# Performance work log

Measured on AMD Instinct MI355X. Metric: run time of the kernel, lower is better.

The kernel has to match this reference:

```python
import jax, jax.numpy as jnp
import numpy as np

DIM = 1024
HEADS = 16
DIM_HEAD = 64
INNER = HEADS * DIM_HEAD  # 1024
EPS = 1e-5


def setup_inputs() -> dict:
    key = jax.random.key(0)
    ks = jax.random.split(key, 5)
    x = jax.random.normal(ks[0], (4, 2048, DIM), dtype=jnp.float32)
    ln_gamma = jnp.ones((DIM,), dtype=jnp.float32)
    ln_beta = jnp.zeros((DIM,), dtype=jnp.float32)
    # nn.Linear weights ~ U(-1/sqrt(fan_in), 1/sqrt(fan_in)); stored as (out, in) in torch,
    # here kept as (in, out) for x @ W.
    lim = 1.0 / np.sqrt(DIM)
    w_qkv = jax.random.uniform(ks[1], (DIM, 3 * INNER), minval=-lim, maxval=lim, dtype=jnp.float32)
    lim2 = 1.0 / np.sqrt(INNER)
    w_out = jax.random.uniform(ks[2], (INNER, DIM), minval=-lim2, maxval=lim2, dtype=jnp.float32)
    return {"x": x, "ln_gamma": ln_gamma, "ln_beta": ln_beta, "w_qkv": w_qkv, "w_out": w_out}


def reference(x, ln_gamma, ln_beta, w_qkv, w_out):
    b, n, d = x.shape
    # LayerNorm
    mu = jnp.mean(x, axis=-1, keepdims=True)
    var = jnp.mean(jnp.square(x - mu), axis=-1, keepdims=True)
    xn = (x - mu) * jax.lax.rsqrt(var + EPS) * ln_gamma + ln_beta
    # QKV projection
    qkv = xn @ w_qkv  # (b, n, 3*inner)
    q, k, v = jnp.split(qkv, 3, axis=-1)
    def to_heads(t):
        return t.reshape(b, n, HEADS, DIM_HEAD).transpose(0, 2, 1, 3)  # (b,h,n,dh)
    q, k, v = to_heads(q), to_heads(k), to_heads(v)
    scale = DIM_HEAD ** -0.5
    scores = jnp.einsum('bhqd,bhkd->bhqk', q, k) * scale
    causal = jnp.tril(jnp.ones((n, n), dtype=bool))
    scores = jnp.where(causal, scores, -jnp.inf)
    probs = jax.nn.softmax(scores, axis=-1)
    out = jnp.einsum('bhqk,bhkd->bhqd', probs, v)
    out = out.transpose(0, 2, 1, 3).reshape(b, n, INNER)
    return out @ w_out
```

## Files before the change

kernel.cpp:

```cpp
#include <hip/hip_runtime.h>
#include <hip/hip_bf16.h>

#define DIM 1024
#define HEADS 16
#define DH 64
#define SEQ 2048
#define BATCH 4
#define ROWS (BATCH * SEQ)
#define NQKV (3 * DIM)

typedef __attribute__((ext_vector_type(8))) __bf16 bf16x8;
typedef __attribute__((ext_vector_type(4))) __bf16 bf16x4;
typedef __attribute__((ext_vector_type(4))) float f32x4;

__device__ inline void gload16(const void* g, void* l) {
  __builtin_amdgcn_global_load_lds(
      (const __attribute__((address_space(1))) void*)g,
      (__attribute__((address_space(3))) void*)l, 16, 0, 0);
}

__device__ inline float fast_exp2(float x) {
#if __has_builtin(__builtin_amdgcn_exp2f)
  return __builtin_amdgcn_exp2f(x);
#else
  return exp2f(x);
#endif
}

__global__ __launch_bounds__(256) void ln_kernel(
    const float* __restrict__ x, const float* __restrict__ gamma,
    const float* __restrict__ beta, __bf16* __restrict__ xnb) {
  const int row = blockIdx.x;
  const int tid = threadIdx.x;
  const float4* xr = (const float4*)(x + (size_t)row * DIM);
  float4 v = xr[tid];
  float s1 = v.x + v.y + v.z + v.w;
  float s2 = v.x * v.x + v.y * v.y + v.z * v.z + v.w * v.w;
#pragma unroll
  for (int d = 32; d > 0; d >>= 1) {
    s1 += __shfl_xor(s1, d);
    s2 += __shfl_xor(s2, d);
  }
  __shared__ float red1[4], red2[4];
  const int wave = tid >> 6, lane = tid & 63;
  if (lane == 0) { red1[wave] = s1; red2[wave] = s2; }
  __syncthreads();
  s1 = red1[0] + red1[1] + red1[2] + red1[3];
  s2 = red2[0] + red2[1] + red2[2] + red2[3];
  const float mean = s1 * (1.0f / DIM);
  const float var = s2 * (1.0f / DIM) - mean * mean;
  const float rstd = rsqrtf(var + 1e-5f);
  float4 g = ((const float4*)gamma)[tid];
  float4 b = ((const float4*)beta)[tid];
  bf16x4 o;
  o[0] = (__bf16)((v.x - mean) * rstd * g.x + b.x);
  o[1] = (__bf16)((v.y - mean) * rstd * g.y + b.y);
  o[2] = (__bf16)((v.z - mean) * rstd * g.z + b.z);
  o[3] = (__bf16)((v.w - mean) * rstd * g.w + b.w);
  *(bf16x4*)(xnb + (size_t)row * DIM + tid * 4) = o;
}

__global__ __launch_bounds__(256) void transpose_cast(
    const float* __restrict__ in, __bf16* __restrict__ outT, int rows, int cols) {
  __shared__ float tile[32][33];
  const int tx = threadIdx.x & 31, ty = threadIdx.x >> 5;
  const int c0 = blockIdx.x * 32, r0 = blockIdx.y * 32;
#pragma unroll
  for (int rr = ty; rr < 32; rr += 8)
    tile[rr][tx] = in[(size_t)(r0 + rr) * cols + c0 + tx];
  __syncthreads();
#pragma unroll
  for (int rr = ty; rr < 32; rr += 8)
    outT[(size_t)(c0 + rr) * rows + r0 + tx] = (__bf16)tile[tx][rr];
}

template <int MODE>
__global__ __launch_bounds__(256) void gemm128(
    const __bf16* __restrict__ A, const __bf16* __restrict__ Bt, int K, int N,
    float* __restrict__ Cout, __bf16* __restrict__ qb, __bf16* __restrict__ kb,
    __bf16* __restrict__ vtb) {
  __shared__ __bf16 As[2][128 * 32];
  __shared__ __bf16 Bs[2][128 * 32];
  const int tid = threadIdx.x;
  const int wave = tid >> 6, lane = tid & 63;
  const int quad = lane >> 4, l16 = lane & 15;
  const int wm = wave >> 1, wn = wave & 1;
  const size_t tileM = (size_t)blockIdx.x * 128;
  const size_t tileN = (size_t)blockIdx.y * 128;
  const int sel = (MODE == 1) ? (int)(tileN >> 10) : 0;
  const bool vmode = (MODE == 1) && (sel == 2);

  f32x4 acc[4][4];
#pragma unroll
  for (int i = 0; i < 4; ++i)
#pragma unroll
    for (int j = 0; j < 4; ++j) acc[i][j] = (f32x4){0.f, 0.f, 0.f, 0.f};

  const int sr = lane >> 2;
  const int sc = lane & 3;
  const int ck = (l16 >> 1) & 3;

  const __bf16* Abase = A + tileM * (size_t)K;
  const __bf16* Bbase = Bt + tileN * (size_t)K;

  auto stage = [&](int buf, int k0) {
#pragma unroll
    for (int p = 0; p < 2; ++p) {
      const int rbase = p * 64 + wave * 16;
      const int row = rbase + sr;
      const int gc = (sc ^ ((row >> 1) & 3)) << 3;
      gload16(Abase + (size_t)row * K + k0 + gc, &As[buf][rbase * 32]);
      gload16(Bbase + (size_t)row * K + k0 + gc, &Bs[buf][rbase * 32]);
    }
  };

  const int NIT = K >> 5;
  stage(0, 0);
  for (int it = 0; it < NIT; ++it) {
    __syncthreads();
    if (it + 1 < NIT) stage((it + 1) & 1, (it + 1) << 5);
    const int buf = it & 1;
    bf16x8 af[4], bfr[4];
#pragma unroll
    for (int mt = 0; mt < 4; ++mt)
      af[mt] =
          *(const bf16x8*)&As[buf][(wm * 64 + mt * 16 + l16) * 32 + ((quad ^ ck) << 3)];
#pragma unroll
    for (int nt = 0; nt < 4; ++nt)
      bfr[nt] =
          *(const bf16x8*)&Bs[buf][(wn * 64 + nt * 16 + l16) * 32 + ((quad ^ ck) << 3)];
    if (vmode) {
#pragma unroll
      for (int mt = 0; mt < 4; ++mt)
#pragma unroll
        for (int nt = 0; nt < 4; ++nt)
          acc[mt][nt] = __builtin_amdgcn_mfma_f32_16x16x32_bf16(af[mt], bfr[nt],
                                                                acc[mt][nt], 0, 0, 0);
    } else {
#pragma unroll
      for (int mt = 0; mt < 4; ++mt)
#pragma unroll
        for (int nt = 0; nt < 4; ++nt)
          acc[mt][nt] = __builtin_amdgcn_mfma_f32_16x16x32_bf16(bfr[nt], af[mt],
                                                                acc[mt][nt], 0, 0, 0);
    }
  }

  if (MODE == 0) {
#pragma unroll
    for (int mt = 0; mt < 4; ++mt) {
      const size_t m = tileM + wm * 64 + mt * 16 + l16;
#pragma unroll
      for (int nt = 0; nt < 4; ++nt) {
        const size_t n0 = tileN + wn * 64 + nt * 16 + quad * 4;
        *(f32x4*)&Cout[m * (size_t)N + n0] = acc[mt][nt];
      }
    }
  } else if (sel < 2) {
    __bf16* dst = (sel == 0) ? qb : kb;
#pragma unroll
    for (int mt = 0; mt < 4; ++mt) {
      const size_t m = tileM + wm * 64 + mt * 16 + l16;
      const int b = (int)(m >> 11), seq = (int)(m & 2047);
#pragma unroll
      for (int nt = 0; nt < 4; ++nt) {
        const int c = (int)(tileN & 1023) + wn * 64 + nt * 16 + quad * 4;
        const int head = c >> 6, dh = c & 63;
        bf16x4 pk;
#pragma unroll
        for (int r = 0; r < 4; ++r) pk[r] = (__bf16)acc[mt][nt][r];
        *(bf16x4*)&dst[(((size_t)b * HEADS + head) * SEQ + seq) * DH + dh] = pk;
      }
    }
  } else {
#pragma unroll
    for (int nt = 0; nt < 4; ++nt) {
      const int c = (int)(tileN & 1023) + wn * 64 + nt * 16 + l16;
      const int head = c >> 6, dh = c & 63;
#pragma unroll
      for (int mt = 0; mt < 4; ++mt) {
        const size_t m0 = tileM + wm * 64 + mt * 16 + quad * 4;
        const int b = (int)(m0 >> 11), seq = (int)(m0 & 2047);
        bf16x4 pk;
#pragma unroll
        for (int r = 0; r < 4; ++r) pk[r] = (__bf16)acc[mt][nt][r];
        *(bf16x4*)&vtb[(((size_t)b * HEADS + head) * DH + dh) * SEQ + seq] = pk;
      }
    }
  }
}

__global__ __launch_bounds__(256, 4) void attn_kernel(
    const __bf16* __restrict__ qb, const __bf16* __restrict__ kb,
    const __bf16* __restrict__ vtb, __bf16* __restrict__ ob) {
  const int bh = blockIdx.x;
  const int by = blockIdx.y;
  const int tid = threadIdx.x;
  const int wave = tid >> 6, lane = tid & 63;
  const int quad = lane >> 4, l16 = lane & 15;

  __shared__ __bf16 Ks[2][64 * 64];
  __shared__ __bf16 Vs[2][64 * 64];
  __shared__ __bf16 Ps[4][16 * 36];

  const __bf16* kg = kb + (size_t)bh * SEQ * DH;
  const __bf16* vg = vtb + (size_t)bh * DH * SEQ;

  const int i1 = by, i2 = 31 - by;
  const int T = 33;

  const int kr = lane >> 3, kc = lane & 7;

  auto stage = [&](int buf, int j) {
#pragma unroll
    for (int p = 0; p < 2; ++p) {
      const int rbase = wave * 16 + p * 8;
      const int row = rbase + kr;
      gload16(kg + (size_t)(j * 64 + row) * DH + ((kc ^ (row & 7)) << 3),
              &Ks[buf][rbase * 64]);
      gload16(vg + (size_t)row * SEQ + j * 64 + ((kc ^ (row & 7)) << 3),
              &Vs[buf][rbase * 64]);
    }
  };

  const float QSCALE = 0.125f * 1.44269504088896f;
  bf16x8 qf[2];
  auto load_q = [&](int i) {
    const __bf16* qbase = qb + ((size_t)bh * SEQ + (size_t)i * 64 + wave * 16) * DH;
#pragma unroll
    for (int ks = 0; ks < 2; ++ks) {
      bf16x8 v = *(const bf16x8*)(qbase + l16 * DH + ks * 32 + quad * 8);
#pragma unroll
      for (int e = 0; e < 8; ++e) v[e] = (__bf16)((float)v[e] * QSCALE);
      qf[ks] = v;
    }
  };

  float m_i, l_i;
  f32x4 o_acc[4];
  auto reset_state = [&]() {
    m_i = -1e30f;
    l_i = 0.f;
#pragma unroll
    for (int md = 0; md < 4; ++md) o_acc[md] = (f32x4){0.f, 0.f, 0.f, 0.f};
  };
  const int b_out = bh >> 4, h_out = bh & 15;
  auto epilogue = [&](int i) {
    float lsum = l_i;
    lsum += __shfl_xor(lsum, 16);
    lsum += __shfl_xor(lsum, 32);
    const float inv = __builtin_amdgcn_rcpf(lsum);
    const int seq = i * 64 + wave * 16 + l16;
    __bf16* dst = ob + ((size_t)b_out * SEQ + seq) * DIM + h_out * DH;
#pragma unroll
    for (int md = 0; md < 4; ++md) {
      bf16x4 pk;
#pragma unroll
      for (int r = 0; r < 4; ++r) pk[r] = (__bf16)(o_acc[md][r] * inv);
      *(bf16x4*)(dst + md * 16 + quad * 4) = pk;
    }
  };

  load_q(i1);
  reset_state();
  stage(0, 0);

  for (int t = 0; t < T; ++t) {
    __syncthreads();
    if (t + 1 < T) {
      const int jn = (t + 1 <= by) ? (t + 1) : (t - by);
      stage((t + 1) & 1, jn);
    }
    const int buf = t & 1;
    const int i = (t <= by) ? i1 : i2;
    const int j = (t <= by) ? t : (t - by - 1);
    const bool diag = (j == i);

    f32x4 sa[4];
#pragma unroll
    for (int nt = 0; nt < 4; ++nt) sa[nt] = (f32x4){0.f, 0.f, 0.f, 0.f};
#pragma unroll
    for (int nt = 0; nt < 4; ++nt)
#pragma unroll
      for (int ks = 0; ks < 2; ++ks) {
        bf16x8 kf = *(const bf16x8*)&Ks[buf][(nt * 16 + l16) * 64 +
                                            (((ks * 4 + quad) ^ (l16 & 7)) << 3)];
        sa[nt] = __builtin_amdgcn_mfma_f32_16x16x32_bf16(kf, qf[ks], sa[nt], 0, 0, 0);
      }

    if (diag) {
      const int qrl = wave * 16 + l16;
#pragma unroll
      for (int nt = 0; nt < 4; ++nt)
#pragma unroll
        for (int r = 0; r < 4; ++r) {
          const int kvl = nt * 16 + quad * 4 + r;
          if (kvl > qrl) sa[nt][r] = -1e30f;
        }
    }

    {
      float mx = -1e30f;
#pragma unroll
      for (int nt = 0; nt < 4; ++nt)
#pragma unroll
        for (int r = 0; r < 4; ++r) mx = fmaxf(mx, sa[nt][r]);
      mx = fmaxf(mx, __shfl_xor(mx, 16));
      mx = fmaxf(mx, __shfl_xor(mx, 32));
      const float mnew = fmaxf(m_i, mx);
      const float alpha = fast_exp2(m_i - mnew);
      m_i = mnew;
      float rs = 0.f;
#pragma unroll
      for (int nt = 0; nt < 4; ++nt)
#pragma unroll
        for (int r = 0; r < 4; ++r) {
          const float p = fast_exp2(sa[nt][r] - mnew);
          sa[nt][r] = p;
          rs += p;
        }
      l_i = l_i * alpha + rs;
#pragma unroll
      for (int md = 0; md < 4; ++md)
#pragma unroll
        for (int r = 0; r < 4; ++r) o_acc[md][r] *= alpha;
    }

#pragma unroll
    for (int c = 0; c < 2; ++c) {
#pragma unroll
      for (int ntl = 0; ntl < 2; ++ntl) {
        const int nt = c * 2 + ntl;
        bf16x4 pk;
#pragma unroll
        for (int r = 0; r < 4; ++r) pk[r] = (__bf16)sa[nt][r];
        *(bf16x4*)&Ps[wave][l16 * 36 + ntl * 16 + quad * 4] = pk;
      }
      bf16x8 pf = *(const bf16x8*)&Ps[wave][l16 * 36 + quad * 8];
#pragma unroll
      for (int md = 0; md < 4; ++md) {
        bf16x8 vf = *(const bf16x8*)&Vs[buf][(md * 16 + l16) * 64 +
                                            (((c * 4 + quad) ^ (l16 & 7)) << 3)];
        o_acc[md] = __builtin_amdgcn_mfma_f32_16x16x32_bf16(vf, pf, o_acc[md], 0, 0, 0);
      }
    }

    if (t == by) {
      epilogue(i1);
      reset_state();
      load_q(i2);
    }
  }
  epilogue(i2);
}

extern "C" void kernel_launch(void* const* d_in, const int* in_sizes, int n_in,
                              void* d_out, int out_size, void* d_ws, size_t ws_size,
                              hipStream_t stream) {
  const float* x = (const float*)d_in[0];
  const float* gamma = (const float*)d_in[1];
  const float* beta = (const float*)d_in[2];
  const float* w_qkv = (const float*)d_in[3];
  const float* w_out = (const float*)d_in[4];
  float* out = (float*)d_out;

  char* ws = (char*)d_ws;
  const size_t MB = 1024 * 1024;
  __bf16* xnb = (__bf16*)ws;
  __bf16* wqkvT = (__bf16*)(ws + 16 * MB);
  __bf16* woutT = (__bf16*)(ws + 24 * MB);
  __bf16* qbuf = (__bf16*)(ws + 32 * MB);
  __bf16* kbuf = (__bf16*)(ws + 48 * MB);
  __bf16* vtbuf = (__bf16*)(ws + 64 * MB);
  __bf16* attnb = xnb;

  ln_kernel<<<ROWS, 256, 0, stream>>>(x, gamma, beta, xnb);
  transpose_cast<<<dim3(NQKV / 32, DIM / 32), 256, 0, stream>>>(w_qkv, wqkvT, DIM, NQKV);
  transpose_cast<<<dim3(DIM / 32, DIM / 32), 256, 0, stream>>>(w_out, woutT, DIM, DIM);
  gemm128<1><<<dim3(ROWS / 128, NQKV / 128), 256, 0, stream>>>(
      xnb, wqkvT, DIM, NQKV, nullptr, qbuf, kbuf, vtbuf);
  attn_kernel<<<dim3(BATCH * HEADS, 16), 256, 0, stream>>>(qbuf, kbuf, vtbuf, attnb);
  gemm128<0><<<dim3(ROWS / 128, DIM / 128), 256, 0, stream>>>(
      attnb, woutT, DIM, DIM, out, nullptr, nullptr, nullptr);
}
```

Before: 285.0 us.

## Rewrite projection GEMMs as 256x256 tiles with 4-stage pipeline and XCD swizzle

Replaces the 128x128 two-buffer GEMM with a 256x256 tile using 512 threads, four LDS stages with explicit vmcnt waits, and staggered A/B staging split around two MFMA halves. Block indices are remapped so consecutive tiles land on the same XCD for L2 reuse, and setprio raises MFMA priority. The larger tile raises arithmetic intensity, but LDS use (128KB) and register pressure grow and the grid shrinks to 384/128 blocks, which risks poor occupancy and tail effects.

```diff
diff --git a/kernel.cpp b/kernel.cpp
--- a/kernel.cpp
+++ b/kernel.cpp
@@ -75,81 +75,145 @@
 }
 
 template <int MODE>
-__global__ __launch_bounds__(256) void gemm128(
-    const __bf16* __restrict__ A, const __bf16* __restrict__ Bt, int K, int N,
-    float* __restrict__ Cout, __bf16* __restrict__ qb, __bf16* __restrict__ kb,
-    __bf16* __restrict__ vtb) {
-  __shared__ __bf16 As[2][128 * 32];
-  __shared__ __bf16 Bs[2][128 * 32];
+__global__ __launch_bounds__(512, 2) void gemm256(
+    const __bf16* __restrict__ A, const __bf16* __restrict__ Bt, const int K,
+    const int N, float* __restrict__ Cout, __bf16* __restrict__ qb,
+    __bf16* __restrict__ kb, __bf16* __restrict__ vtb) {
+  __shared__ __bf16 As[4][256 * 32];
+  __shared__ __bf16 Bs[4][256 * 32];
   const int tid = threadIdx.x;
   const int wave = tid >> 6, lane = tid & 63;
   const int quad = lane >> 4, l16 = lane & 15;
-  const int wm = wave >> 1, wn = wave & 1;
-  const size_t tileM = (size_t)blockIdx.x * 128;
-  const size_t tileN = (size_t)blockIdx.y * 128;
+  const int wm = wave >> 2, wn = wave & 3;
+
+  const int cpx = gridDim.x >> 3;
+  const int wg = ((int)blockIdx.x & 7) * cpx + ((int)blockIdx.x >> 3);
+  const int MT = ROWS / 256;
+  const size_t tileM = (size_t)(wg % MT) * 256;
+  const size_t tileN = (size_t)(wg / MT) * 256;
   const int sel = (MODE == 1) ? (int)(tileN >> 10) : 0;
   const bool vmode = (MODE == 1) && (sel == 2);
 
-  f32x4 acc[4][4];
-#pragma unroll
-  for (int i = 0; i < 4; ++i)
+  f32x4 acc[8][4];
+#pragma unroll
+  for (int i = 0; i < 8; ++i)
 #pragma unroll
     for (int j = 0; j < 4; ++j) acc[i][j] = (f32x4){0.f, 0.f, 0.f, 0.f};
 
   const int sr = lane >> 2;
   const int sc = lane & 3;
   const int ck = (l16 >> 1) & 3;
+  const int coff = (quad ^ ck) << 3;
 
   const __bf16* Abase = A + tileM * (size_t)K;
   const __bf16* Bbase = Bt + tileN * (size_t)K;
 
-  auto stage = [&](int buf, int k0) {
+  auto stageA = [&](int buf, int k0) {
 #pragma unroll
     for (int p = 0; p < 2; ++p) {
-      const int rbase = p * 64 + wave * 16;
+      const int rbase = (wave * 2 + p) * 16;
       const int row = rbase + sr;
       const int gc = (sc ^ ((row >> 1) & 3)) << 3;
       gload16(Abase + (size_t)row * K + k0 + gc, &As[buf][rbase * 32]);
+    }
+  };
+  auto stageB = [&](int buf, int k0) {
+#pragma unroll
+    for (int p = 0; p < 2; ++p) {
+      const int rbase = (wave * 2 + p) * 16;
+      const int row = rbase + sr;
+      const int gc = (sc ^ ((row >> 1) & 3)) << 3;
       gload16(Bbase + (size_t)row * K + k0 + gc, &Bs[buf][rbase * 32]);
     }
   };
 
-  const int NIT = K >> 5;
-  stage(0, 0);
-  for (int it = 0; it < NIT; ++it) {
-    __syncthreads();
-    if (it + 1 < NIT) stage((it + 1) & 1, (it + 1) << 5);
-    const int buf = it & 1;
-    bf16x8 af[4], bfr[4];
-#pragma unroll
-    for (int mt = 0; mt < 4; ++mt)
-      af[mt] =
-          *(const bf16x8*)&As[buf][(wm * 64 + mt * 16 + l16) * 32 + ((quad ^ ck) << 3)];
+  const int NT = K >> 5;
+  stageA(0, 0);
+  stageB(0, 0);
+  stageA(1, 32);
+  stageB(1, 32);
+  stageA(2, 64);
+  stageB(2, 64);
+
+  for (int t = 0; t < NT; ++t) {
+    if (t < NT - 2)
+      asm volatile("s_waitcnt vmcnt(8)" ::: "memory");
+    else if (t < NT - 1)
+      asm volatile("s_waitcnt vmcnt(4)" ::: "memory");
+    else
+      asm volatile("s_waitcnt vmcnt(0)" ::: "memory");
+    __builtin_amdgcn_s_barrier();
+    asm volatile("" ::: "memory");
+    __builtin_amdgcn_sched_barrier(0);
+
+    const int buf = t & 3;
+    const int sbuf = (t + 3) & 3;
+    const bool do_stage = (t + 3 < NT);
+    const int k3 = (t + 3) << 5;
+
+    if (do_stage) stageA(sbuf, k3);
+    bf16x8 bfr[4];
 #pragma unroll
     for (int nt = 0; nt < 4; ++nt)
-      bfr[nt] =
-          *(const bf16x8*)&Bs[buf][(wn * 64 + nt * 16 + l16) * 32 + ((quad ^ ck) << 3)];
-    if (vmode) {
+      bfr[nt] = *(const bf16x8*)&Bs[buf][(wn * 64 + nt * 16 + l16) * 32 + coff];
+    {
+      bf16x8 af[4];
 #pragma unroll
       for (int mt = 0; mt < 4; ++mt)
-#pragma unroll
-        for (int nt = 0; nt < 4; ++nt)
-          acc[mt][nt] = __builtin_amdgcn_mfma_f32_16x16x32_bf16(af[mt], bfr[nt],
-                                                                acc[mt][nt], 0, 0, 0);
-    } else {
+        af[mt] = *(const bf16x8*)&As[buf][(wm * 128 + mt * 16 + l16) * 32 + coff];
+      __builtin_amdgcn_s_setprio(1);
+      if (vmode) {
+#pragma unroll
+        for (int mt = 0; mt < 4; ++mt)
+#pragma unroll
+          for (int nt = 0; nt < 4; ++nt)
+            acc[mt][nt] = __builtin_amdgcn_mfma_f32_16x16x32_bf16(
+                af[mt], bfr[nt], acc[mt][nt], 0, 0, 0);
+      } else {
+#pragma unroll
+        for (int mt = 0; mt < 4; ++mt)
+#pragma unroll
+          for (int nt = 0; nt < 4; ++nt)
+            acc[mt][nt] = __builtin_amdgcn_mfma_f32_16x16x32_bf16(
+                bfr[nt], af[mt], acc[mt][nt], 0, 0, 0);
+      }
+      __builtin_amdgcn_s_setprio(0);
+    }
+    __builtin_amdgcn_s_barrier();
+    asm volatile("" ::: "memory");
+    __builtin_amdgcn_sched_barrier(0);
+
+    if (do_stage) stageB(sbuf, k3);
+    {
+      bf16x8 af[4];
 #pragma unroll
       for (int mt = 0; mt < 4; ++mt)
-#pragma unroll
-        for (int nt = 0; nt < 4; ++nt)
-          acc[mt][nt] = __builtin_amdgcn_mfma_f32_16x16x32_bf16(bfr[nt], af[mt],
-                                                                acc[mt][nt], 0, 0, 0);
+        af[mt] =
+            *(const bf16x8*)&As[buf][(wm * 128 + (mt + 4) * 16 + l16) * 32 + coff];
+      __builtin_amdgcn_s_setprio(1);
+      if (vmode) {
+#pragma unroll
+        for (int mt = 0; mt < 4; ++mt)
+#pragma unroll
+          for (int nt = 0; nt < 4; ++nt)
+            acc[mt + 4][nt] = __builtin_amdgcn_mfma_f32_16x16x32_bf16(
+                af[mt], bfr[nt], acc[mt + 4][nt], 0, 0, 0);
+      } else {
+#pragma unroll
+        for (int mt = 0; mt < 4; ++mt)
+#pragma unroll
+          for (int nt = 0; nt < 4; ++nt)
+            acc[mt + 4][nt] = __builtin_amdgcn_mfma_f32_16x16x32_bf16(
+                bfr[nt], af[mt], acc[mt + 4][nt], 0, 0, 0);
+      }
+      __builtin_amdgcn_s_setprio(0);
     }
   }
 
   if (MODE == 0) {
 #pragma unroll
-    for (int mt = 0; mt < 4; ++mt) {
-      const size_t m = tileM + wm * 64 + mt * 16 + l16;
+    for (int mt = 0; mt < 8; ++mt) {
+      const size_t m = tileM + wm * 128 + mt * 16 + l16;
 #pragma unroll
       for (int nt = 0; nt < 4; ++nt) {
         const size_t n0 = tileN + wn * 64 + nt * 16 + quad * 4;
@@ -159,8 +223,8 @@
   } else if (sel < 2) {
     __bf16* dst = (sel == 0) ? qb : kb;
 #pragma unroll
-    for (int mt = 0; mt < 4; ++mt) {
-      const size_t m = tileM + wm * 64 + mt * 16 + l16;
+    for (int mt = 0; mt < 8; ++mt) {
+      const size_t m = tileM + wm * 128 + mt * 16 + l16;
       const int b = (int)(m >> 11), seq = (int)(m & 2047);
 #pragma unroll
       for (int nt = 0; nt < 4; ++nt) {
@@ -178,8 +242,8 @@
       const int c = (int)(tileN & 1023) + wn * 64 + nt * 16 + l16;
       const int head = c >> 6, dh = c & 63;
 #pragma unroll
-      for (int mt = 0; mt < 4; ++mt) {
-        const size_t m0 = tileM + wm * 64 + mt * 16 + quad * 4;
+      for (int mt = 0; mt < 8; ++mt) {
+        const size_t m0 = tileM + wm * 128 + mt * 16 + quad * 4;
         const int b = (int)(m0 >> 11), seq = (int)(m0 & 2047);
         bf16x4 pk;
 #pragma unroll
@@ -377,9 +441,9 @@
   ln_kernel<<<ROWS, 256, 0, stream>>>(x, gamma, beta, xnb);
   transpose_cast<<<dim3(NQKV / 32, DIM / 32), 256, 0, stream>>>(w_qkv, wqkvT, DIM, NQKV);
   transpose_cast<<<dim3(DIM / 32, DIM / 32), 256, 0, stream>>>(w_out, woutT, DIM, DIM);
-  gemm128<1><<<dim3(ROWS / 128, NQKV / 128), 256, 0, stream>>>(
+  gemm256<1><<<dim3((ROWS / 256) * (NQKV / 256)), 512, 0, stream>>>(
       xnb, wqkvT, DIM, NQKV, nullptr, qbuf, kbuf, vtbuf);
   attn_kernel<<<dim3(BATCH * HEADS, 16), 256, 0, stream>>>(qbuf, kbuf, vtbuf, attnb);
-  gemm128<0><<<dim3(ROWS / 128, DIM / 128), 256, 0, stream>>>(
+  gemm256<0><<<dim3((ROWS / 256) * (DIM / 256)), 512, 0, stream>>>(
       attnb, woutT, DIM, DIM, out, nullptr, nullptr, nullptr);
 }
```

Result: slower. 375.0 us (+31.6%).
